# Optimization experiments

Hardware: AMD Instinct MI355X
Metric: run time of the kernel (lower is better)

Reference implementation:

```python
import jax, jax.numpy as jnp
import numpy as np

D = 128
N_A = 50000
N_B = 50000
E = 600000
EPS = 1e-5

def setup_inputs() -> dict:
    key = jax.random.key(0)
    ks = jax.random.split(key, 16)
    s = 1.0 / np.sqrt(D)
    inp = {
        "x_A": jax.random.normal(ks[0], (N_A, D), jnp.float32),
        "x_B": jax.random.normal(ks[1], (N_B, D), jnp.float32),
        "ei_aa": jax.random.randint(ks[2], (2, E), 0, N_A),
        "ei_ba": jnp.stack([jax.random.randint(ks[3], (E,), 0, N_B),
                             jax.random.randint(ks[4], (E,), 0, N_A)]),
        "ei_ab": jnp.stack([jax.random.randint(ks[5], (E,), 0, N_A),
                             jax.random.randint(ks[6], (E,), 0, N_B)]),
        # SAGEConv params per edge type: W_l (neighbor), W_r (root), bias
        "W_l_aa": jax.random.uniform(ks[7], (D, D), jnp.float32, -s, s),
        "W_r_aa": jax.random.uniform(ks[8], (D, D), jnp.float32, -s, s),
        "b_aa": jnp.zeros((D,), jnp.float32),
        "W_l_ba": jax.random.uniform(ks[9], (D, D), jnp.float32, -s, s),
        "W_r_ba": jax.random.uniform(ks[10], (D, D), jnp.float32, -s, s),
        "b_ba": jnp.zeros((D,), jnp.float32),
        "W_l_ab": jax.random.uniform(ks[11], (D, D), jnp.float32, -s, s),
        "W_r_ab": jax.random.uniform(ks[12], (D, D), jnp.float32, -s, s),
        "b_ab": jnp.zeros((D,), jnp.float32),
        "gamma": jnp.ones((D,), jnp.float32),
        "beta": jnp.zeros((D,), jnp.float32),
    }
    return inp

def _sage(x_src, x_dst, ei, W_l, W_r, b, n_dst):
    # mean aggregation of gathered neighbor features (0 for isolated nodes, like PyG)
    msgs = x_src[ei[0]]                                            # [E, D]
    ssum = jax.ops.segment_sum(msgs, ei[1], num_segments=n_dst)    # [n_dst, D]
    cnt = jax.ops.segment_sum(jnp.ones((ei.shape[1], 1), x_src.dtype), ei[1], num_segments=n_dst)
    mean = ssum / jnp.maximum(cnt, 1.0)
    return mean @ W_l.T + x_dst @ W_r.T + b

def _layernorm(x, gamma, beta):
    mu = jnp.mean(x, axis=-1, keepdims=True)
    var = jnp.mean(jnp.square(x - mu), axis=-1, keepdims=True)
    return (x - mu) * jax.lax.rsqrt(var + EPS) * gamma + beta

def reference(x_A, x_B, ei_aa, ei_ba, ei_ab,
              W_l_aa, W_r_aa, b_aa, W_l_ba, W_r_ba, b_ba,
              W_l_ab, W_r_ab, b_ab, gamma, beta):
    # HeteroConv(aggr='sum'): sum conv outputs per destination node type
    out_A = (_sage(x_A, x_A, ei_aa, W_l_aa, W_r_aa, b_aa, N_A)
             + _sage(x_B, x_A, ei_ba, W_l_ba, W_r_ba, b_ba, N_A))
    out_B = _sage(x_A, x_B, ei_ab, W_l_ab, W_r_ab, b_ab, N_B)
    out_A = jax.nn.relu(_layernorm(out_A, gamma, beta))
    out_B = jax.nn.relu(_layernorm(out_B, gamma, beta))
    return out_A, out_B
```

## Files before the change

kernel.cpp:

```cpp
#include <hip/hip_runtime.h>

#define NNODE 50000
#define NEDGE 600000
#define NDST 150000
#define NEALL 1800000
#define NBKT 586
#define EPB 16384
#define P5B 110
#define ECAP 8192

typedef __attribute__((ext_vector_type(8))) __bf16 bf16x8;
typedef __attribute__((ext_vector_type(4))) float f32x4;
typedef __attribute__((ext_vector_type(4))) unsigned int u32x4;

__device__ int dtype_of(const void* gamma) {
    unsigned int g = *(const unsigned int*)gamma;
    if (g == 0x3F803F80u) return 0;
    if (g == 0x3C003C00u) return 1;
    return 2;
}

__device__ float bf2f(unsigned short u) {
    unsigned int x = ((unsigned int)u) << 16;
    float f;
    __builtin_memcpy(&f, &x, 4);
    return f;
}

__device__ float bflo(unsigned int w) {
    unsigned int x = w << 16;
    float f;
    __builtin_memcpy(&f, &x, 4);
    return f;
}
__device__ float bfhi(unsigned int w) {
    unsigned int x = w & 0xFFFF0000u;
    float f;
    __builtin_memcpy(&f, &x, 4);
    return f;
}

__device__ unsigned short f2bf(float f) {
    unsigned int x;
    __builtin_memcpy(&x, &f, 4);
    unsigned int r = (x + 0x7FFFu + ((x >> 16) & 1u)) >> 16;
    return (unsigned short)r;
}

__device__ float ldf(const void* p, int i, int dt) {
    if (dt == 0) return bf2f(((const unsigned short*)p)[i]);
    if (dt == 1) return (float)(((const _Float16*)p)[i]);
    return ((const float*)p)[i];
}

__device__ void stf(void* p, int i, int dt, float v) {
    if (dt == 0) ((unsigned short*)p)[i] = f2bf(v);
    else if (dt == 1) ((_Float16*)p)[i] = (_Float16)v;
    else ((float*)p)[i] = v;
}

__device__ void edge4(const int* ei_aa, const int* ei_ba, const int* ei_ab,
                      int e, int4* d4, int4* s4) {
    const int* dbase;
    const int* sbase;
    int add;
    if (e < NEDGE) { sbase = ei_aa + e; dbase = ei_aa + NEDGE + e; add = 0; }
    else if (e < 2 * NEDGE) {
        int ee = e - NEDGE;
        sbase = ei_ba + ee; dbase = ei_ba + NEDGE + ee; add = 50000;
    } else {
        int ee = e - 2 * NEDGE;
        sbase = ei_ab + ee; dbase = ei_ab + NEDGE + ee; add = 100000;
    }
    int4 d = *(const int4*)dbase;
    d.x += add; d.y += add; d.z += add; d.w += add;
    *d4 = d;
    *s4 = *(const int4*)sbase;
}

__global__ __launch_bounds__(1024) void p5_sort(
    const int* ei_aa, const int* ei_ba, const int* ei_ab,
    unsigned int* blkBuf, int* bbCnt, int* ibOfs) {
    __shared__ int cnt[NBKT];
    __shared__ int ls[1024];
    __shared__ unsigned int buf[EPB];
    int t = threadIdx.x;
    int4 dreg[4], sreg[4];
    bool val[4];
    int e0 = blockIdx.x * EPB + t * 16;
#pragma unroll
    for (int u = 0; u < 4; ++u) {
        int e = e0 + u * 4;
        val[u] = e < NEALL;
        if (val[u]) edge4(ei_aa, ei_ba, ei_ab, e, &dreg[u], &sreg[u]);
    }
    if (t < NBKT) cnt[t] = 0;
    __syncthreads();
#pragma unroll
    for (int u = 0; u < 4; ++u) {
        if (val[u]) {
            atomicAdd(&cnt[dreg[u].x >> 8], 1);
            atomicAdd(&cnt[dreg[u].y >> 8], 1);
            atomicAdd(&cnt[dreg[u].z >> 8], 1);
            atomicAdd(&cnt[dreg[u].w >> 8], 1);
        }
    }
    __syncthreads();
    int v = (t < NBKT) ? cnt[t] : 0;
    ls[t] = v;
    __syncthreads();
    for (int o = 1; o < 1024; o <<= 1) {
        int add = (t >= o) ? ls[t - o] : 0;
        __syncthreads();
        ls[t] += add;
        __syncthreads();
    }
    if (t < NBKT) {
        int excl = ls[t] - v;
        bbCnt[blockIdx.x * NBKT + t] = v;
        ibOfs[blockIdx.x * NBKT + t] = excl;
        cnt[t] = excl;
    }
    __syncthreads();
#pragma unroll
    for (int u = 0; u < 4; ++u) {
        if (val[u]) {
            int dv[4] = {dreg[u].x, dreg[u].y, dreg[u].z, dreg[u].w};
            int sv[4] = {sreg[u].x, sreg[u].y, sreg[u].z, sreg[u].w};
#pragma unroll
            for (int w = 0; w < 4; ++w) {
                int bkt = dv[w] >> 8;
                int r = atomicAdd(&cnt[bkt], 1);
                buf[r] = ((unsigned int)(dv[w] & 255) << 16) | (unsigned int)sv[w];
            }
        }
    }
    __syncthreads();
    unsigned int* dst = blkBuf + blockIdx.x * EPB;
#pragma unroll
    for (int u = 0; u < 4; ++u) {
        int idx = t * 16 + u * 4;
        *(u32x4*)&dst[idx] = *(const u32x4*)&buf[idx];
    }
}

__global__ void p2_colsum(const int* bbCnt, int* colSum) {
    int wave = threadIdx.x >> 6;
    int lane = threadIdx.x & 63;
    int j = blockIdx.x * 4 + wave;
    if (j >= NBKT) return;
    int s = 0;
    if (lane < P5B) s += bbCnt[lane * NBKT + j];
    if (lane + 64 < P5B) s += bbCnt[(lane + 64) * NBKT + j];
    for (int o = 1; o < 64; o <<= 1) s += __shfl_xor(s, o);
    if (lane == 0) colSum[j] = s;
}

__global__ void p3_scan(const int* colSum, int* bucketStart) {
    __shared__ int ls[1024];
    int t = threadIdx.x;
    int v = (t < NBKT) ? colSum[t] : 0;
    ls[t] = v;
    __syncthreads();
    for (int o = 1; o < 1024; o <<= 1) {
        int add = (t >= o) ? ls[t - o] : 0;
        __syncthreads();
        ls[t] += add;
        __syncthreads();
    }
    if (t < NBKT) bucketStart[t] = ls[t] - v;
    if (t == 0) bucketStart[NBKT] = NEALL;
}

__device__ unsigned int rd_entry(const unsigned int* blkBuf, const int* rp,
                                 const int* runSrc, int i) {
    int lo = 0, hi = P5B - 1;
    while (lo < hi) {
        int m = (lo + hi) >> 1;
        if (rp[m] > i) hi = m;
        else lo = m + 1;
    }
    int base = lo ? rp[lo - 1] : 0;
    return blkBuf[runSrc[lo] + (i - base)];
}

__global__ __launch_bounds__(256) void p6_fine(
    const unsigned int* blkBuf, const int* bbCnt, const int* ibOfs,
    const int* bucketStart, int* rowStart, int* edgeSrc) {
    __shared__ int rp[128];
    __shared__ int runSrc[P5B];
    __shared__ unsigned int ebuf[ECAP];
    __shared__ int h[256];
    __shared__ int s[256];
    __shared__ int cur[256];
    int t = threadIdx.x;
    int j = blockIdx.x;
    int lo = bucketStart[j];
    int tot = bucketStart[j + 1] - lo;

    if (t < 128) {
        int c = (t < P5B) ? bbCnt[t * NBKT + j] : 0;
        rp[t] = c;
        if (t < P5B) runSrc[t] = t * EPB + ibOfs[t * NBKT + j];
    }
    __syncthreads();
    for (int o = 1; o < 128; o <<= 1) {
        int add = (t < 128 && t >= o) ? rp[t - o] : 0;
        __syncthreads();
        if (t < 128) rp[t] += add;
        __syncthreads();
    }

    bool staged = tot <= ECAP;
    if (staged) {
        for (int i = t; i < tot; i += 256)
            ebuf[i] = rd_entry(blkBuf, rp, runSrc, i);
    }
    h[t] = 0;
    __syncthreads();
    for (int i = t; i < tot; i += 256) {
        unsigned int w = staged ? ebuf[i] : rd_entry(blkBuf, rp, runSrc, i);
        atomicAdd(&h[w >> 16], 1);
    }
    __syncthreads();
    s[t] = h[t];
    __syncthreads();
    for (int o = 1; o < 256; o <<= 1) {
        int add = (t >= o) ? s[t - o] : 0;
        __syncthreads();
        s[t] += add;
        __syncthreads();
    }
    int excl = s[t] - h[t];
    int dst = j * 256 + t;
    if (dst < NDST) rowStart[dst] = lo + excl;
    if (j == NBKT - 1 && t == 0) rowStart[NDST] = NEALL;
    cur[t] = lo + excl;
    __syncthreads();
    for (int i = t; i < tot; i += 256) {
        unsigned int w = staged ? ebuf[i] : rd_entry(blkBuf, rp, runSrc, i);
        int pos = atomicAdd(&cur[w >> 16], 1);
        edgeSrc[pos] = (int)(w & 0xFFFFu);
    }
}

__global__ __launch_bounds__(256) void gather3_kernel(
    const void* x_A, const void* x_B, const int* rowStart, const int* edgeSrc,
    unsigned short* mean1, unsigned short* mean2, unsigned short* mean3,
    const void* gam) {
    int dt = dtype_of(gam);
    int wave = threadIdx.x >> 6;
    int lane = threadIdx.x & 63;
    int d = blockIdx.x * 4 + wave;
    if (d >= NDST) return;
    const void* x;
    unsigned short* mean;
    int node;
    if (d < 50000) { x = x_A; mean = mean1; node = d; }
    else if (d < 100000) { x = x_B; mean = mean2; node = d - 50000; }
    else { x = x_A; mean = mean3; node = d - 100000; }

    int beg = rowStart[d];
    int end = rowStart[d + 1];

    if (dt == 0) {
        const u32x4* xq = (const u32x4*)x;
        int sub = lane >> 4;
        int col = lane & 15;
        float a[8];
#pragma unroll
        for (int j = 0; j < 8; ++j) a[j] = 0.0f;

        for (int i = beg; i < end; i += 8) {
            int e0 = i + sub;
            int e1 = i + 4 + sub;
            bool p0 = e0 < end;
            bool p1 = e1 < end;
            int s0 = edgeSrc[p0 ? e0 : beg];
            int s1 = edgeSrc[p1 ? e1 : beg];
            u32x4 w0 = xq[s0 * 16 + col];
            u32x4 w1 = xq[s1 * 16 + col];
            if (!p0) w0 = u32x4{0u, 0u, 0u, 0u};
            if (!p1) w1 = u32x4{0u, 0u, 0u, 0u};
            a[0] += bflo(w0.x) + bflo(w1.x);
            a[1] += bfhi(w0.x) + bfhi(w1.x);
            a[2] += bflo(w0.y) + bflo(w1.y);
            a[3] += bfhi(w0.y) + bfhi(w1.y);
            a[4] += bflo(w0.z) + bflo(w1.z);
            a[5] += bfhi(w0.z) + bfhi(w1.z);
            a[6] += bflo(w0.w) + bflo(w1.w);
            a[7] += bfhi(w0.w) + bfhi(w1.w);
        }
#pragma unroll
        for (int j = 0; j < 8; ++j) {
            a[j] += __shfl_xor(a[j], 16);
            a[j] += __shfl_xor(a[j], 32);
        }
        float inv = (end > beg) ? 1.0f / (float)(end - beg) : 0.0f;
        if (lane < 16) {
            u32x4 o;
            o.x = (unsigned int)f2bf(a[0] * inv) | ((unsigned int)f2bf(a[1] * inv) << 16);
            o.y = (unsigned int)f2bf(a[2] * inv) | ((unsigned int)f2bf(a[3] * inv) << 16);
            o.z = (unsigned int)f2bf(a[4] * inv) | ((unsigned int)f2bf(a[5] * inv) << 16);
            o.w = (unsigned int)f2bf(a[6] * inv) | ((unsigned int)f2bf(a[7] * inv) << 16);
            ((u32x4*)mean)[node * 16 + lane] = o;
        }
    } else {
        float a0 = 0.0f, a1 = 0.0f;
        for (int i = beg; i < end; ++i) {
            int src = edgeSrc[i];
            a0 += ldf(x, src * 128 + 2 * lane, dt);
            a1 += ldf(x, src * 128 + 2 * lane + 1, dt);
        }
        float inv = (end > beg) ? 1.0f / (float)(end - beg) : 0.0f;
        unsigned int lo = f2bf(a0 * inv);
        unsigned int hi = f2bf(a1 * inv);
        ((unsigned int*)mean)[node * 64 + lane] = lo | (hi << 16);
    }
}

__global__ void prep_kernel(const void* Wl_aa, const void* Wr_aa, const void* b_aa,
                            const void* Wl_ba, const void* Wr_ba, const void* b_ba,
                            const void* Wl_ab, const void* Wr_ab, const void* b_ab,
                            unsigned short* WA, unsigned short* WB,
                            float* biasA, float* biasB, const void* gam) {
    int dt = dtype_of(gam);
    int idx = blockIdx.x * 256 + threadIdx.x;
    if (idx < 49152) {
        int n = idx / 384;
        int k = idx % 384;
        float v;
        if (k < 128) v = ldf(Wl_aa, n * 128 + k, dt);
        else if (k < 256) v = ldf(Wl_ba, n * 128 + k - 128, dt);
        else v = ldf(Wr_aa, n * 128 + k - 256, dt) + ldf(Wr_ba, n * 128 + k - 256, dt);
        WA[idx] = f2bf(v);
    } else if (idx < 49152 + 32768) {
        int i = idx - 49152;
        int n = i / 256;
        int k = i % 256;
        float v;
        if (k < 128) v = ldf(Wl_ab, n * 128 + k, dt);
        else v = ldf(Wr_ab, n * 128 + k - 128, dt);
        WB[i] = f2bf(v);
    } else if (idx < 49152 + 32768 + 128) {
        int j = idx - (49152 + 32768);
        biasA[j] = ldf(b_aa, j, dt) + ldf(b_ba, j, dt);
    } else if (idx < 49152 + 32768 + 256) {
        int j = idx - (49152 + 32768 + 128);
        biasB[j] = ldf(b_ab, j, dt);
    }
}

__device__ bf16x8 pack8(const float* f) {
    unsigned short u[8];
    for (int j = 0; j < 8; ++j) u[j] = f2bf(f[j]);
    bf16x8 r;
    __builtin_memcpy(&r, u, 16);
    return r;
}

template <int KTOT>
__device__ bf16x8 loadA(const unsigned short* mean1, const unsigned short* mean2,
                        const void* x, int r, int k, int dt) {
    if (k < 128) {
        return *(const bf16x8*)(mean1 + r * 128 + k);
    }
    if (KTOT == 384 && k < 256) {
        return *(const bf16x8*)(mean2 + r * 128 + (k - 128));
    }
    int kx = k - (KTOT - 128);
    if (dt == 0) {
        return *(const bf16x8*)((const unsigned short*)x + r * 128 + kx);
    }
    float f[8];
    for (int j = 0; j < 8; ++j) f[j] = ldf(x, r * 128 + kx + j, dt);
    return pack8(f);
}

template <int KTOT>
__device__ void gemm_body(int bx, const unsigned short* mean1,
                          const unsigned short* mean2, const void* x,
                          const unsigned short* Wu, const float* bias,
                          const void* gam, const void* bet, void* out,
                          int rowOff, int dt) {
    int lane = threadIdx.x & 63;
    int wave = threadIdx.x >> 6;
    int q16 = lane >> 4;
    int l16 = lane & 15;
    int mBase = (bx * 4 + wave) * 32;

    int r0 = mBase + l16;
    int r1 = mBase + 16 + l16;
    if (r0 > NNODE - 1) r0 = NNODE - 1;
    if (r1 > NNODE - 1) r1 = NNODE - 1;

    f32x4 acc[2][8];
    for (int rt = 0; rt < 2; ++rt)
        for (int tt = 0; tt < 8; ++tt) acc[rt][tt] = f32x4{0.f, 0.f, 0.f, 0.f};

    const int NCH = KTOT / 32;
    for (int ck = 0; ck < NCH; ++ck) {
        int k = ck * 32 + q16 * 8;
        bf16x8 a0 = loadA<KTOT>(mean1, mean2, x, r0, k, dt);
        bf16x8 a1 = loadA<KTOT>(mean1, mean2, x, r1, k, dt);
#pragma unroll
        for (int tt = 0; tt < 8; ++tt) {
            int n = tt * 16 + l16;
            bf16x8 b = *(const bf16x8*)(Wu + n * KTOT + k);
            acc[0][tt] = __builtin_amdgcn_mfma_f32_16x16x32_bf16(a0, b, acc[0][tt], 0, 0, 0);
            acc[1][tt] = __builtin_amdgcn_mfma_f32_16x16x32_bf16(a1, b, acc[1][tt], 0, 0, 0);
        }
    }

    float g[8], be[8], bs[8];
    for (int tt = 0; tt < 8; ++tt) {
        int j = tt * 16 + l16;
        g[tt] = ldf(gam, j, dt);
        be[tt] = ldf(bet, j, dt);
        bs[tt] = bias[j];
    }

    for (int rt = 0; rt < 2; ++rt) {
        for (int q = 0; q < 4; ++q) {
            int row = mBase + rt * 16 + q16 * 4 + q;
            float v[8];
            float s = 0.f, ss = 0.f;
            for (int tt = 0; tt < 8; ++tt) {
                v[tt] = acc[rt][tt][q] + bs[tt];
                s += v[tt];
                ss += v[tt] * v[tt];
            }
            for (int off = 1; off <= 8; off <<= 1) {
                s += __shfl_xor(s, off);
                ss += __shfl_xor(ss, off);
            }
            float m = s * (1.0f / 128.0f);
            float var = ss * (1.0f / 128.0f) - m * m;
            float rstd = rsqrtf(var + 1e-5f);
            if (row < NNODE) {
                for (int tt = 0; tt < 8; ++tt) {
                    float o = (v[tt] - m) * rstd * g[tt] + be[tt];
                    if (o < 0.0f) o = 0.0f;
                    stf(out, (rowOff + row) * 128 + tt * 16 + l16, dt, o);
                }
            }
        }
    }
}

__global__ __launch_bounds__(256) void gemm_ln_all(
    const unsigned short* mean1, const unsigned short* mean2,
    const unsigned short* mean3, const void* x_A, const void* x_B,
    const unsigned short* WA, const unsigned short* WB,
    const float* bA, const float* bB,
    const void* gam, const void* bet, void* out) {
    int dt = dtype_of(gam);
    if (blockIdx.x < 391)
        gemm_body<384>(blockIdx.x, mean1, mean2, x_A, WA, bA, gam, bet, out, 0, dt);
    else
        gemm_body<256>(blockIdx.x - 391, mean3, nullptr, x_B, WB, bB, gam, bet, out,
                       NNODE, dt);
}

extern "C" void kernel_launch(void* const* d_in, const int* in_sizes, int n_in,
                              void* d_out, int out_size, void* d_ws, size_t ws_size,
                              hipStream_t stream) {
    const void* x_A = d_in[0];
    const void* x_B = d_in[1];
    const int* ei_aa = (const int*)d_in[2];
    const int* ei_ba = (const int*)d_in[3];
    const int* ei_ab = (const int*)d_in[4];
    const void* W_l_aa = d_in[5];
    const void* W_r_aa = d_in[6];
    const void* b_aa = d_in[7];
    const void* W_l_ba = d_in[8];
    const void* W_r_ba = d_in[9];
    const void* b_ba = d_in[10];
    const void* W_l_ab = d_in[11];
    const void* W_r_ab = d_in[12];
    const void* b_ab = d_in[13];
    const void* gam = d_in[14];
    const void* bet = d_in[15];

    unsigned short* mean1 = (unsigned short*)d_ws;
    unsigned short* mean2 = mean1 + 6400000;
    unsigned short* mean3 = mean2 + 6400000;
    unsigned short* WA = mean3 + 6400000;
    unsigned short* WB = WA + 49152;
    float* bA = (float*)(WB + 32768);
    float* bB = bA + 128;
    int* bbCnt = (int*)(bB + 128);
    int* ibOfs = bbCnt + P5B * NBKT;
    int* colSum = ibOfs + P5B * NBKT;
    int* bucketStart = colSum + NBKT;
    int* rowStart = bucketStart + NBKT + 1;
    int* edgeSrc = rowStart + NDST + 1;
    unsigned int* blkBuf = (unsigned int*)mean1;

    prep_kernel<<<322, 256, 0, stream>>>(W_l_aa, W_r_aa, b_aa, W_l_ba, W_r_ba, b_ba,
                                         W_l_ab, W_r_ab, b_ab, WA, WB, bA, bB, gam);

    p5_sort<<<P5B, 1024, 0, stream>>>(ei_aa, ei_ba, ei_ab, blkBuf, bbCnt, ibOfs);
    p2_colsum<<<147, 256, 0, stream>>>(bbCnt, colSum);
    p3_scan<<<1, 1024, 0, stream>>>(colSum, bucketStart);
    p6_fine<<<NBKT, 256, 0, stream>>>(blkBuf, bbCnt, ibOfs, bucketStart,
                                      rowStart, edgeSrc);

    gather3_kernel<<<37500, 256, 0, stream>>>(x_A, x_B, rowStart, edgeSrc,
                                              mean1, mean2, mean3, gam);

    gemm_ln_all<<<782, 256, 0, stream>>>(mean1, mean2, mean3, x_A, x_B,
                                         WA, WB, bA, bB, gam, bet, d_out);
}
```

Measured before the change: 461.1 us.

## Fuse neighbor-mean gather into GEMM+LayerNorm via LDS, merge colsum into scan

```diff
diff --git a/kernel.cpp b/kernel.cpp
--- a/kernel.cpp
+++ b/kernel.cpp
@@ -8,6 +8,8 @@
 #define EPB 16384
 #define P5B 110
 #define ECAP 8192
+#define NPB 128
+#define FBN 391
 
 typedef __attribute__((ext_vector_type(8))) __bf16 bf16x8;
 typedef __attribute__((ext_vector_type(4))) float f32x4;
@@ -144,22 +146,13 @@
     }
 }
 
-__global__ void p2_colsum(const int* bbCnt, int* colSum) {
-    int wave = threadIdx.x >> 6;
-    int lane = threadIdx.x & 63;
-    int j = blockIdx.x * 4 + wave;
-    if (j >= NBKT) return;
-    int s = 0;
-    if (lane < P5B) s += bbCnt[lane * NBKT + j];
-    if (lane + 64 < P5B) s += bbCnt[(lane + 64) * NBKT + j];
-    for (int o = 1; o < 64; o <<= 1) s += __shfl_xor(s, o);
-    if (lane == 0) colSum[j] = s;
-}
-
-__global__ void p3_scan(const int* colSum, int* bucketStart) {
+__global__ void p23_scan(const int* bbCnt, int* bucketStart) {
     __shared__ int ls[1024];
     int t = threadIdx.x;
-    int v = (t < NBKT) ? colSum[t] : 0;
+    int v = 0;
+    if (t < NBKT) {
+        for (int b = 0; b < P5B; ++b) v += bbCnt[b * NBKT + t];
+    }
     ls[t] = v;
     __syncthreads();
     for (int o = 1; o < 1024; o <<= 1) {
@@ -241,81 +234,6 @@
         unsigned int w = staged ? ebuf[i] : rd_entry(blkBuf, rp, runSrc, i);
         int pos = atomicAdd(&cur[w >> 16], 1);
         edgeSrc[pos] = (int)(w & 0xFFFFu);
-    }
-}
-
-__global__ __launch_bounds__(256) void gather3_kernel(
-    const void* x_A, const void* x_B, const int* rowStart, const int* edgeSrc,
-    unsigned short* mean1, unsigned short* mean2, unsigned short* mean3,
-    const void* gam) {
-    int dt = dtype_of(gam);
-    int wave = threadIdx.x >> 6;
-    int lane = threadIdx.x & 63;
-    int d = blockIdx.x * 4 + wave;
-    if (d >= NDST) return;
-    const void* x;
-    unsigned short* mean;
-    int node;
-    if (d < 50000) { x = x_A; mean = mean1; node = d; }
-    else if (d < 100000) { x = x_B; mean = mean2; node = d - 50000; }
-    else { x = x_A; mean = mean3; node = d - 100000; }
-
-    int beg = rowStart[d];
-    int end = rowStart[d + 1];
-
-    if (dt == 0) {
-        const u32x4* xq = (const u32x4*)x;
-        int sub = lane >> 4;
-        int col = lane & 15;
-        float a[8];
-#pragma unroll
-        for (int j = 0; j < 8; ++j) a[j] = 0.0f;
-
-        for (int i = beg; i < end; i += 8) {
-            int e0 = i + sub;
-            int e1 = i + 4 + sub;
-            bool p0 = e0 < end;
-            bool p1 = e1 < end;
-            int s0 = edgeSrc[p0 ? e0 : beg];
-            int s1 = edgeSrc[p1 ? e1 : beg];
-            u32x4 w0 = xq[s0 * 16 + col];
-            u32x4 w1 = xq[s1 * 16 + col];
-            if (!p0) w0 = u32x4{0u, 0u, 0u, 0u};
-            if (!p1) w1 = u32x4{0u, 0u, 0u, 0u};
-            a[0] += bflo(w0.x) + bflo(w1.x);
-            a[1] += bfhi(w0.x) + bfhi(w1.x);
-            a[2] += bflo(w0.y) + bflo(w1.y);
-            a[3] += bfhi(w0.y) + bfhi(w1.y);
-            a[4] += bflo(w0.z) + bflo(w1.z);
-            a[5] += bfhi(w0.z) + bfhi(w1.z);
-            a[6] += bflo(w0.w) + bflo(w1.w);
-            a[7] += bfhi(w0.w) + bfhi(w1.w);
-        }
-#pragma unroll
-        for (int j = 0; j < 8; ++j) {
-            a[j] += __shfl_xor(a[j], 16);
-            a[j] += __shfl_xor(a[j], 32);
-        }
-        float inv = (end > beg) ? 1.0f / (float)(end - beg) : 0.0f;
-        if (lane < 16) {
-            u32x4 o;
-            o.x = (unsigned int)f2bf(a[0] * inv) | ((unsigned int)f2bf(a[1] * inv) << 16);
-            o.y = (unsigned int)f2bf(a[2] * inv) | ((unsigned int)f2bf(a[3] * inv) << 16);
-            o.z = (unsigned int)f2bf(a[4] * inv) | ((unsigned int)f2bf(a[5] * inv) << 16);
-            o.w = (unsigned int)f2bf(a[6] * inv) | ((unsigned int)f2bf(a[7] * inv) << 16);
-            ((u32x4*)mean)[node * 16 + lane] = o;
-        }
-    } else {
-        float a0 = 0.0f, a1 = 0.0f;
-        for (int i = beg; i < end; ++i) {
-            int src = edgeSrc[i];
-            a0 += ldf(x, src * 128 + 2 * lane, dt);
-            a1 += ldf(x, src * 128 + 2 * lane + 1, dt);
-        }
-        float inv = (end > beg) ? 1.0f / (float)(end - beg) : 0.0f;
-        unsigned int lo = f2bf(a0 * inv);
-        unsigned int hi = f2bf(a1 * inv);
-        ((unsigned int*)mean)[node * 64 + lane] = lo | (hi << 16);
     }
 }
 
@@ -360,59 +278,51 @@
 }
 
 template <int KTOT>
-__device__ bf16x8 loadA(const unsigned short* mean1, const unsigned short* mean2,
-                        const void* x, int r, int k, int dt) {
-    if (k < 128) {
-        return *(const bf16x8*)(mean1 + r * 128 + k);
-    }
-    if (KTOT == 384 && k < 256) {
-        return *(const bf16x8*)(mean2 + r * 128 + (k - 128));
-    }
-    int kx = k - (KTOT - 128);
-    if (dt == 0) {
-        return *(const bf16x8*)((const unsigned short*)x + r * 128 + kx);
-    }
-    float f[8];
-    for (int j = 0; j < 8; ++j) f[j] = ldf(x, r * 128 + kx + j, dt);
-    return pack8(f);
-}
-
-template <int KTOT>
-__device__ void gemm_body(int bx, const unsigned short* mean1,
-                          const unsigned short* mean2, const void* x,
-                          const unsigned short* Wu, const float* bias,
-                          const void* gam, const void* bet, void* out,
-                          int rowOff, int dt) {
+__device__ void fused_gemm(const unsigned short* meanLds, const void* x,
+                           const unsigned short* Wu, const float* bias,
+                           const void* gam, const void* bet, void* out,
+                           int n0, int rowOff, int dt) {
+    const int KMEAN = KTOT - 128;
     int lane = threadIdx.x & 63;
     int wave = threadIdx.x >> 6;
     int q16 = lane >> 4;
     int l16 = lane & 15;
-    int mBase = (bx * 4 + wave) * 32;
-
-    int r0 = mBase + l16;
-    int r1 = mBase + 16 + l16;
-    if (r0 > NNODE - 1) r0 = NNODE - 1;
-    if (r1 > NNODE - 1) r1 = NNODE - 1;
-
-    f32x4 acc[2][8];
-    for (int rt = 0; rt < 2; ++rt)
-        for (int tt = 0; tt < 8; ++tt) acc[rt][tt] = f32x4{0.f, 0.f, 0.f, 0.f};
+    int rL = wave * 16 + l16;
+    int xrow = n0 + rL;
+    if (xrow > NNODE - 1) xrow = NNODE - 1;
+
+    f32x4 acc[8];
+#pragma unroll
+    for (int tt = 0; tt < 8; ++tt) acc[tt] = f32x4{0.f, 0.f, 0.f, 0.f};
 
     const int NCH = KTOT / 32;
+#pragma unroll
     for (int ck = 0; ck < NCH; ++ck) {
         int k = ck * 32 + q16 * 8;
-        bf16x8 a0 = loadA<KTOT>(mean1, mean2, x, r0, k, dt);
-        bf16x8 a1 = loadA<KTOT>(mean1, mean2, x, r1, k, dt);
+        bf16x8 a0;
+        if (k < KMEAN) {
+            int bo = (rL * 512 + k * 2) ^ ((rL & 7) << 4);
+            a0 = *(const bf16x8*)((const char*)meanLds + bo);
+        } else {
+            int kx = k - KMEAN;
+            if (dt == 0) {
+                a0 = *(const bf16x8*)((const unsigned short*)x + xrow * 128 + kx);
+            } else {
+                float f[8];
+                for (int j = 0; j < 8; ++j) f[j] = ldf(x, xrow * 128 + kx + j, dt);
+                a0 = pack8(f);
+            }
+        }
 #pragma unroll
         for (int tt = 0; tt < 8; ++tt) {
             int n = tt * 16 + l16;
             bf16x8 b = *(const bf16x8*)(Wu + n * KTOT + k);
-            acc[0][tt] = __builtin_amdgcn_mfma_f32_16x16x32_bf16(a0, b, acc[0][tt], 0, 0, 0);
-            acc[1][tt] = __builtin_amdgcn_mfma_f32_16x16x32_bf16(a1, b, acc[1][tt], 0, 0, 0);
+            acc[tt] = __builtin_amdgcn_mfma_f32_16x16x32_bf16(a0, b, acc[tt], 0, 0, 0);
         }
     }
 
     float g[8], be[8], bs[8];
+#pragma unroll
     for (int tt = 0; tt < 8; ++tt) {
         int j = tt * 16 + l16;
         g[tt] = ldf(gam, j, dt);
@@ -420,46 +330,129 @@
         bs[tt] = bias[j];
     }
 
-    for (int rt = 0; rt < 2; ++rt) {
-        for (int q = 0; q < 4; ++q) {
-            int row = mBase + rt * 16 + q16 * 4 + q;
-            float v[8];
-            float s = 0.f, ss = 0.f;
+    for (int q = 0; q < 4; ++q) {
+        int rowL = wave * 16 + q16 * 4 + q;
+        float v[8];
+        float s = 0.f, ss = 0.f;
+#pragma unroll
+        for (int tt = 0; tt < 8; ++tt) {
+            v[tt] = acc[tt][q] + bs[tt];
+            s += v[tt];
+            ss += v[tt] * v[tt];
+        }
+        for (int off = 1; off <= 8; off <<= 1) {
+            s += __shfl_xor(s, off);
+            ss += __shfl_xor(ss, off);
+        }
+        float m = s * (1.0f / 128.0f);
+        float var = ss * (1.0f / 128.0f) - m * m;
+        float rstd = rsqrtf(var + 1e-5f);
+        int grow = n0 + rowL;
+        if (grow < NNODE) {
+#pragma unroll
             for (int tt = 0; tt < 8; ++tt) {
-                v[tt] = acc[rt][tt][q] + bs[tt];
-                s += v[tt];
-                ss += v[tt] * v[tt];
+                float o = (v[tt] - m) * rstd * g[tt] + be[tt];
+                if (o < 0.0f) o = 0.0f;
+                stf(out, (rowOff + grow) * 128 + tt * 16 + l16, dt, o);
             }
-            for (int off = 1; off <= 8; off <<= 1) {
-                s += __shfl_xor(s, off);
-                ss += __shfl_xor(ss, off);
-            }
-            float m = s * (1.0f / 128.0f);
-            float var = ss * (1.0f / 128.0f) - m * m;
-            float rstd = rsqrtf(var + 1e-5f);
-            if (row < NNODE) {
-                for (int tt = 0; tt < 8; ++tt) {
-                    float o = (v[tt] - m) * rstd * g[tt] + be[tt];
-                    if (o < 0.0f) o = 0.0f;
-                    stf(out, (rowOff + row) * 128 + tt * 16 + l16, dt, o);
-                }
-            }
-        }
-    }
-}
-
-__global__ __launch_bounds__(256) void gemm_ln_all(
-    const unsigned short* mean1, const unsigned short* mean2,
-    const unsigned short* mean3, const void* x_A, const void* x_B,
+        }
+    }
+}
+
+__global__ __launch_bounds__(512, 4) void fused_gg(
+    const void* x_A, const void* x_B, const int* rowStart, const int* edgeSrc,
     const unsigned short* WA, const unsigned short* WB,
     const float* bA, const float* bB,
     const void* gam, const void* bet, void* out) {
+    __shared__ unsigned short meanLds[NPB * 256];
     int dt = dtype_of(gam);
-    if (blockIdx.x < 391)
-        gemm_body<384>(blockIdx.x, mean1, mean2, x_A, WA, bA, gam, bet, out, 0, dt);
+    bool typeB = blockIdx.x >= FBN;
+    int bx = typeB ? blockIdx.x - FBN : blockIdx.x;
+    int n0 = bx * NPB;
+    int wave = threadIdx.x >> 6;
+    int lane = threadIdx.x & 63;
+    int sub = lane >> 4;
+    int col = lane & 15;
+
+    int nlists = typeB ? NPB : 2 * NPB;
+    for (int L = wave; L < nlists; L += 8) {
+        int node, part, dstIdx, row;
+        const void* x;
+        if (!typeB) {
+            node = n0 + (L >> 1);
+            part = L & 1;
+            dstIdx = part ? 50000 + node : node;
+            x = part ? x_B : x_A;
+            row = L >> 1;
+        } else {
+            node = n0 + L;
+            part = 0;
+            dstIdx = 100000 + node;
+            x = x_A;
+            row = L;
+        }
+
+        float a[8];
+#pragma unroll
+        for (int j = 0; j < 8; ++j) a[j] = 0.0f;
+        int deg = 0;
+        if (node < NNODE) {
+            int beg = rowStart[dstIdx];
+            int end = rowStart[dstIdx + 1];
+            deg = end - beg;
+            if (dt == 0) {
+                const u32x4* xq = (const u32x4*)x;
+                for (int i = beg; i < end; i += 8) {
+                    int e0 = i + sub;
+                    int e1 = i + 4 + sub;
+                    bool p0 = e0 < end;
+                    bool p1 = e1 < end;
+                    int s0 = edgeSrc[p0 ? e0 : beg];
+                    int s1 = edgeSrc[p1 ? e1 : beg];
+                    u32x4 w0 = xq[s0 * 16 + col];
+                    u32x4 w1 = xq[s1 * 16 + col];
+                    if (!p0) w0 = u32x4{0u, 0u, 0u, 0u};
+                    if (!p1) w1 = u32x4{0u, 0u, 0u, 0u};
+                    a[0] += bflo(w0.x) + bflo(w1.x);
+                    a[1] += bfhi(w0.x) + bfhi(w1.x);
+                    a[2] += bflo(w0.y) + bflo(w1.y);
+                    a[3] += bfhi(w0.y) + bfhi(w1.y);
+                    a[4] += bflo(w0.z) + bflo(w1.z);
+                    a[5] += bfhi(w0.z) + bfhi(w1.z);
+                    a[6] += bflo(w0.w) + bflo(w1.w);
+                    a[7] += bfhi(w0.w) + bfhi(w1.w);
+                }
+            } else {
+                for (int i = beg + sub; i < end; i += 4) {
+                    int src = edgeSrc[i];
+#pragma unroll
+                    for (int j = 0; j < 8; ++j)
+                        a[j] += ldf(x, src * 128 + col * 8 + j, dt);
+                }
+            }
+        }
+#pragma unroll
+        for (int j = 0; j < 8; ++j) {
+            a[j] += __shfl_xor(a[j], 16);
+            a[j] += __shfl_xor(a[j], 32);
+        }
+        float inv = (deg > 0) ? 1.0f / (float)deg : 0.0f;
+        if (lane < 16) {
+            u32x4 o;
+            o.x = (unsigned int)f2bf(a[0] * inv) | ((unsigned int)f2bf(a[1] * inv) << 16);
+            o.y = (unsigned int)f2bf(a[2] * inv) | ((unsigned int)f2bf(a[3] * inv) << 16);
+            o.z = (unsigned int)f2bf(a[4] * inv) | ((unsigned int)f2bf(a[5] * inv) << 16);
+            o.w = (unsigned int)f2bf(a[6] * inv) | ((unsigned int)f2bf(a[7] * inv) << 16);
+            int byteOff = (row * 512 + part * 256 + col * 16) ^ ((row & 7) << 4);
+            *(u32x4*)((char*)meanLds + byteOff) = o;
+        }
+    }
+    __syncthreads();
+
+    if (!typeB)
+        fused_gemm<384>(meanLds, x_A, WA, bA, gam, bet, out, n0, 0, dt);
     else
-        gemm_body<256>(blockIdx.x - 391, mean3, nullptr, x_B, WB, bB, gam, bet, out,
-                       NNODE, dt);
+        fused_gemm<256>(meanLds, x_B, WB, bB, gam, bet, out, n0, NNODE, dt);
 }
 
 extern "C" void kernel_launch(void* const* d_in, const int* in_sizes, int n_in,
@@ -482,33 +475,25 @@
     const void* gam = d_in[14];
     const void* bet = d_in[15];
 
-    unsigned short* mean1 = (unsigned short*)d_ws;
-    unsigned short* mean2 = mean1 + 6400000;
-    unsigned short* mean3 = mean2 + 6400000;
-    unsigned short* WA = mean3 + 6400000;
+    int* bbCnt = (int*)d_ws;
+    int* ibOfs = bbCnt + P5B * NBKT;
+    int* bucketStart = ibOfs + P5B * NBKT;
+    int* rowStart = bucketStart + NBKT + 1;
+    int* edgeSrc = rowStart + NDST + 1;
+    unsigned int* blkBuf = (unsigned int*)(edgeSrc + NEALL);
+    unsigned short* WA = (unsigned short*)(blkBuf + P5B * EPB);
     unsigned short* WB = WA + 49152;
     float* bA = (float*)(WB + 32768);
     float* bB = bA + 128;
-    int* bbCnt = (int*)(bB + 128);
-    int* ibOfs = bbCnt + P5B * NBKT;
-    int* colSum = ibOfs + P5B * NBKT;
-    int* bucketStart = colSum + NBKT;
-    int* rowStart = bucketStart + NBKT + 1;
-    int* edgeSrc = rowStart + NDST + 1;
-    unsigned int* blkBuf = (unsigned int*)mean1;
 
     prep_kernel<<<322, 256, 0, stream>>>(W_l_aa, W_r_aa, b_aa, W_l_ba, W_r_ba, b_ba,
                                          W_l_ab, W_r_ab, b_ab, WA, WB, bA, bB, gam);
 
     p5_sort<<<P5B, 1024, 0, stream>>>(ei_aa, ei_ba, ei_ab, blkBuf, bbCnt, ibOfs);
-    p2_colsum<<<147, 256, 0, stream>>>(bbCnt, colSum);
-    p3_scan<<<1, 1024, 0, stream>>>(colSum, bucketStart);
+    p23_scan<<<1, 1024, 0, stream>>>(bbCnt, bucketStart);
     p6_fine<<<NBKT, 256, 0, stream>>>(blkBuf, bbCnt, ibOfs, bucketStart,
                                       rowStart, edgeSrc);
 
-    gather3_kernel<<<37500, 256, 0, stream>>>(x_A, x_B, rowStart, edgeSrc,
-                                              mean1, mean2, mean3, gam);
-
-    gemm_ln_all<<<782, 256, 0, stream>>>(mean1, mean2, mean3, x_A, x_B,
-                                         WA, WB, bA, bB, gam, bet, d_out);
-}
+    fused_gg<<<2 * FBN, 512, 0, stream>>>(x_A, x_B, rowStart, edgeSrc,
+                                          WA, WB, bA, bB, gam, bet, d_out);
+}
```

Result: slower. 782.4 us (+69.7%).

## Fuse fine sort with neighbor gather and fold weight prep into coarse sort

Applied to the files above, without the earlier changes.

```diff
diff --git a/kernel.cpp b/kernel.cpp
--- a/kernel.cpp
+++ b/kernel.cpp
@@ -4,10 +4,12 @@
 #define NEDGE 600000
 #define NDST 150000
 #define NEALL 1800000
-#define NBKT 586
-#define EPB 16384
-#define P5B 110
-#define ECAP 8192
+#define BSZ 147
+#define NBKT 1021
+#define EPB 8192
+#define P5B 220
+#define PREPB 81
+#define ECAP 3072
 
 typedef __attribute__((ext_vector_type(8))) __bf16 bf16x8;
 typedef __attribute__((ext_vector_type(4))) float f32x4;
@@ -78,254 +80,11 @@
     *s4 = *(const int4*)sbase;
 }
 
-__global__ __launch_bounds__(1024) void p5_sort(
-    const int* ei_aa, const int* ei_ba, const int* ei_ab,
-    unsigned int* blkBuf, int* bbCnt, int* ibOfs) {
-    __shared__ int cnt[NBKT];
-    __shared__ int ls[1024];
-    __shared__ unsigned int buf[EPB];
-    int t = threadIdx.x;
-    int4 dreg[4], sreg[4];
-    bool val[4];
-    int e0 = blockIdx.x * EPB + t * 16;
-#pragma unroll
-    for (int u = 0; u < 4; ++u) {
-        int e = e0 + u * 4;
-        val[u] = e < NEALL;
-        if (val[u]) edge4(ei_aa, ei_ba, ei_ab, e, &dreg[u], &sreg[u]);
-    }
-    if (t < NBKT) cnt[t] = 0;
-    __syncthreads();
-#pragma unroll
-    for (int u = 0; u < 4; ++u) {
-        if (val[u]) {
-            atomicAdd(&cnt[dreg[u].x >> 8], 1);
-            atomicAdd(&cnt[dreg[u].y >> 8], 1);
-            atomicAdd(&cnt[dreg[u].z >> 8], 1);
-            atomicAdd(&cnt[dreg[u].w >> 8], 1);
-        }
-    }
-    __syncthreads();
-    int v = (t < NBKT) ? cnt[t] : 0;
-    ls[t] = v;
-    __syncthreads();
-    for (int o = 1; o < 1024; o <<= 1) {
-        int add = (t >= o) ? ls[t - o] : 0;
-        __syncthreads();
-        ls[t] += add;
-        __syncthreads();
-    }
-    if (t < NBKT) {
-        int excl = ls[t] - v;
-        bbCnt[blockIdx.x * NBKT + t] = v;
-        ibOfs[blockIdx.x * NBKT + t] = excl;
-        cnt[t] = excl;
-    }
-    __syncthreads();
-#pragma unroll
-    for (int u = 0; u < 4; ++u) {
-        if (val[u]) {
-            int dv[4] = {dreg[u].x, dreg[u].y, dreg[u].z, dreg[u].w};
-            int sv[4] = {sreg[u].x, sreg[u].y, sreg[u].z, sreg[u].w};
-#pragma unroll
-            for (int w = 0; w < 4; ++w) {
-                int bkt = dv[w] >> 8;
-                int r = atomicAdd(&cnt[bkt], 1);
-                buf[r] = ((unsigned int)(dv[w] & 255) << 16) | (unsigned int)sv[w];
-            }
-        }
-    }
-    __syncthreads();
-    unsigned int* dst = blkBuf + blockIdx.x * EPB;
-#pragma unroll
-    for (int u = 0; u < 4; ++u) {
-        int idx = t * 16 + u * 4;
-        *(u32x4*)&dst[idx] = *(const u32x4*)&buf[idx];
-    }
-}
-
-__global__ void p2_colsum(const int* bbCnt, int* colSum) {
-    int wave = threadIdx.x >> 6;
-    int lane = threadIdx.x & 63;
-    int j = blockIdx.x * 4 + wave;
-    if (j >= NBKT) return;
-    int s = 0;
-    if (lane < P5B) s += bbCnt[lane * NBKT + j];
-    if (lane + 64 < P5B) s += bbCnt[(lane + 64) * NBKT + j];
-    for (int o = 1; o < 64; o <<= 1) s += __shfl_xor(s, o);
-    if (lane == 0) colSum[j] = s;
-}
-
-__global__ void p3_scan(const int* colSum, int* bucketStart) {
-    __shared__ int ls[1024];
-    int t = threadIdx.x;
-    int v = (t < NBKT) ? colSum[t] : 0;
-    ls[t] = v;
-    __syncthreads();
-    for (int o = 1; o < 1024; o <<= 1) {
-        int add = (t >= o) ? ls[t - o] : 0;
-        __syncthreads();
-        ls[t] += add;
-        __syncthreads();
-    }
-    if (t < NBKT) bucketStart[t] = ls[t] - v;
-    if (t == 0) bucketStart[NBKT] = NEALL;
-}
-
-__device__ unsigned int rd_entry(const unsigned int* blkBuf, const int* rp,
-                                 const int* runSrc, int i) {
-    int lo = 0, hi = P5B - 1;
-    while (lo < hi) {
-        int m = (lo + hi) >> 1;
-        if (rp[m] > i) hi = m;
-        else lo = m + 1;
-    }
-    int base = lo ? rp[lo - 1] : 0;
-    return blkBuf[runSrc[lo] + (i - base)];
-}
-
-__global__ __launch_bounds__(256) void p6_fine(
-    const unsigned int* blkBuf, const int* bbCnt, const int* ibOfs,
-    const int* bucketStart, int* rowStart, int* edgeSrc) {
-    __shared__ int rp[128];
-    __shared__ int runSrc[P5B];
-    __shared__ unsigned int ebuf[ECAP];
-    __shared__ int h[256];
-    __shared__ int s[256];
-    __shared__ int cur[256];
-    int t = threadIdx.x;
-    int j = blockIdx.x;
-    int lo = bucketStart[j];
-    int tot = bucketStart[j + 1] - lo;
-
-    if (t < 128) {
-        int c = (t < P5B) ? bbCnt[t * NBKT + j] : 0;
-        rp[t] = c;
-        if (t < P5B) runSrc[t] = t * EPB + ibOfs[t * NBKT + j];
-    }
-    __syncthreads();
-    for (int o = 1; o < 128; o <<= 1) {
-        int add = (t < 128 && t >= o) ? rp[t - o] : 0;
-        __syncthreads();
-        if (t < 128) rp[t] += add;
-        __syncthreads();
-    }
-
-    bool staged = tot <= ECAP;
-    if (staged) {
-        for (int i = t; i < tot; i += 256)
-            ebuf[i] = rd_entry(blkBuf, rp, runSrc, i);
-    }
-    h[t] = 0;
-    __syncthreads();
-    for (int i = t; i < tot; i += 256) {
-        unsigned int w = staged ? ebuf[i] : rd_entry(blkBuf, rp, runSrc, i);
-        atomicAdd(&h[w >> 16], 1);
-    }
-    __syncthreads();
-    s[t] = h[t];
-    __syncthreads();
-    for (int o = 1; o < 256; o <<= 1) {
-        int add = (t >= o) ? s[t - o] : 0;
-        __syncthreads();
-        s[t] += add;
-        __syncthreads();
-    }
-    int excl = s[t] - h[t];
-    int dst = j * 256 + t;
-    if (dst < NDST) rowStart[dst] = lo + excl;
-    if (j == NBKT - 1 && t == 0) rowStart[NDST] = NEALL;
-    cur[t] = lo + excl;
-    __syncthreads();
-    for (int i = t; i < tot; i += 256) {
-        unsigned int w = staged ? ebuf[i] : rd_entry(blkBuf, rp, runSrc, i);
-        int pos = atomicAdd(&cur[w >> 16], 1);
-        edgeSrc[pos] = (int)(w & 0xFFFFu);
-    }
-}
-
-__global__ __launch_bounds__(256) void gather3_kernel(
-    const void* x_A, const void* x_B, const int* rowStart, const int* edgeSrc,
-    unsigned short* mean1, unsigned short* mean2, unsigned short* mean3,
-    const void* gam) {
-    int dt = dtype_of(gam);
-    int wave = threadIdx.x >> 6;
-    int lane = threadIdx.x & 63;
-    int d = blockIdx.x * 4 + wave;
-    if (d >= NDST) return;
-    const void* x;
-    unsigned short* mean;
-    int node;
-    if (d < 50000) { x = x_A; mean = mean1; node = d; }
-    else if (d < 100000) { x = x_B; mean = mean2; node = d - 50000; }
-    else { x = x_A; mean = mean3; node = d - 100000; }
-
-    int beg = rowStart[d];
-    int end = rowStart[d + 1];
-
-    if (dt == 0) {
-        const u32x4* xq = (const u32x4*)x;
-        int sub = lane >> 4;
-        int col = lane & 15;
-        float a[8];
-#pragma unroll
-        for (int j = 0; j < 8; ++j) a[j] = 0.0f;
-
-        for (int i = beg; i < end; i += 8) {
-            int e0 = i + sub;
-            int e1 = i + 4 + sub;
-            bool p0 = e0 < end;
-            bool p1 = e1 < end;
-            int s0 = edgeSrc[p0 ? e0 : beg];
-            int s1 = edgeSrc[p1 ? e1 : beg];
-            u32x4 w0 = xq[s0 * 16 + col];
-            u32x4 w1 = xq[s1 * 16 + col];
-            if (!p0) w0 = u32x4{0u, 0u, 0u, 0u};
-            if (!p1) w1 = u32x4{0u, 0u, 0u, 0u};
-            a[0] += bflo(w0.x) + bflo(w1.x);
-            a[1] += bfhi(w0.x) + bfhi(w1.x);
-            a[2] += bflo(w0.y) + bflo(w1.y);
-            a[3] += bfhi(w0.y) + bfhi(w1.y);
-            a[4] += bflo(w0.z) + bflo(w1.z);
-            a[5] += bfhi(w0.z) + bfhi(w1.z);
-            a[6] += bflo(w0.w) + bflo(w1.w);
-            a[7] += bfhi(w0.w) + bfhi(w1.w);
-        }
-#pragma unroll
-        for (int j = 0; j < 8; ++j) {
-            a[j] += __shfl_xor(a[j], 16);
-            a[j] += __shfl_xor(a[j], 32);
-        }
-        float inv = (end > beg) ? 1.0f / (float)(end - beg) : 0.0f;
-        if (lane < 16) {
-            u32x4 o;
-            o.x = (unsigned int)f2bf(a[0] * inv) | ((unsigned int)f2bf(a[1] * inv) << 16);
-            o.y = (unsigned int)f2bf(a[2] * inv) | ((unsigned int)f2bf(a[3] * inv) << 16);
-            o.z = (unsigned int)f2bf(a[4] * inv) | ((unsigned int)f2bf(a[5] * inv) << 16);
-            o.w = (unsigned int)f2bf(a[6] * inv) | ((unsigned int)f2bf(a[7] * inv) << 16);
-            ((u32x4*)mean)[node * 16 + lane] = o;
-        }
-    } else {
-        float a0 = 0.0f, a1 = 0.0f;
-        for (int i = beg; i < end; ++i) {
-            int src = edgeSrc[i];
-            a0 += ldf(x, src * 128 + 2 * lane, dt);
-            a1 += ldf(x, src * 128 + 2 * lane + 1, dt);
-        }
-        float inv = (end > beg) ? 1.0f / (float)(end - beg) : 0.0f;
-        unsigned int lo = f2bf(a0 * inv);
-        unsigned int hi = f2bf(a1 * inv);
-        ((unsigned int*)mean)[node * 64 + lane] = lo | (hi << 16);
-    }
-}
-
-__global__ void prep_kernel(const void* Wl_aa, const void* Wr_aa, const void* b_aa,
-                            const void* Wl_ba, const void* Wr_ba, const void* b_ba,
-                            const void* Wl_ab, const void* Wr_ab, const void* b_ab,
-                            unsigned short* WA, unsigned short* WB,
-                            float* biasA, float* biasB, const void* gam) {
-    int dt = dtype_of(gam);
-    int idx = blockIdx.x * 256 + threadIdx.x;
+__device__ void prep_body(int idx, const void* Wl_aa, const void* Wr_aa,
+                          const void* b_aa, const void* Wl_ba, const void* Wr_ba,
+                          const void* b_ba, const void* Wl_ab, const void* Wr_ab,
+                          const void* b_ab, unsigned short* WA, unsigned short* WB,
+                          float* biasA, float* biasB, int dt) {
     if (idx < 49152) {
         int n = idx / 384;
         int k = idx % 384;
@@ -351,6 +110,264 @@
     }
 }
 
+__global__ __launch_bounds__(1024) void p5_sort(
+    const int* ei_aa, const int* ei_ba, const int* ei_ab,
+    unsigned int* blkBuf, int* bbCnt, int* ibOfs,
+    const void* Wl_aa, const void* Wr_aa, const void* b_aa,
+    const void* Wl_ba, const void* Wr_ba, const void* b_ba,
+    const void* Wl_ab, const void* Wr_ab, const void* b_ab,
+    unsigned short* WA, unsigned short* WB,
+    float* biasA, float* biasB, const void* gam) {
+    int t = threadIdx.x;
+    if (blockIdx.x >= P5B) {
+        int dt = dtype_of(gam);
+        int idx = (blockIdx.x - P5B) * 1024 + t;
+        prep_body(idx, Wl_aa, Wr_aa, b_aa, Wl_ba, Wr_ba, b_ba,
+                  Wl_ab, Wr_ab, b_ab, WA, WB, biasA, biasB, dt);
+        return;
+    }
+    __shared__ int cnt[NBKT];
+    __shared__ int ls[1024];
+    __shared__ unsigned int buf[EPB];
+    int4 dreg[2], sreg[2];
+    bool val[2];
+    int e0 = blockIdx.x * EPB + t * 8;
+#pragma unroll
+    for (int u = 0; u < 2; ++u) {
+        int e = e0 + u * 4;
+        val[u] = e < NEALL;
+        if (val[u]) edge4(ei_aa, ei_ba, ei_ab, e, &dreg[u], &sreg[u]);
+    }
+    if (t < NBKT) cnt[t] = 0;
+    __syncthreads();
+#pragma unroll
+    for (int u = 0; u < 2; ++u) {
+        if (val[u]) {
+            atomicAdd(&cnt[dreg[u].x / BSZ], 1);
+            atomicAdd(&cnt[dreg[u].y / BSZ], 1);
+            atomicAdd(&cnt[dreg[u].z / BSZ], 1);
+            atomicAdd(&cnt[dreg[u].w / BSZ], 1);
+        }
+    }
+    __syncthreads();
+    int v = (t < NBKT) ? cnt[t] : 0;
+    ls[t] = v;
+    __syncthreads();
+    for (int o = 1; o < 1024; o <<= 1) {
+        int add = (t >= o) ? ls[t - o] : 0;
+        __syncthreads();
+        ls[t] += add;
+        __syncthreads();
+    }
+    if (t < NBKT) {
+        int excl = ls[t] - v;
+        bbCnt[blockIdx.x * NBKT + t] = v;
+        ibOfs[blockIdx.x * NBKT + t] = excl;
+        cnt[t] = excl;
+    }
+    __syncthreads();
+#pragma unroll
+    for (int u = 0; u < 2; ++u) {
+        if (val[u]) {
+            int dv[4] = {dreg[u].x, dreg[u].y, dreg[u].z, dreg[u].w};
+            int sv[4] = {sreg[u].x, sreg[u].y, sreg[u].z, sreg[u].w};
+#pragma unroll
+            for (int w = 0; w < 4; ++w) {
+                int bkt = dv[w] / BSZ;
+                int dl = dv[w] - bkt * BSZ;
+                int r = atomicAdd(&cnt[bkt], 1);
+                buf[r] = ((unsigned int)dl << 16) | (unsigned int)sv[w];
+            }
+        }
+    }
+    __syncthreads();
+    unsigned int* dst = blkBuf + blockIdx.x * EPB;
+#pragma unroll
+    for (int u = 0; u < 2; ++u) {
+        int idx = t * 8 + u * 4;
+        *(u32x4*)&dst[idx] = *(const u32x4*)&buf[idx];
+    }
+}
+
+__global__ __launch_bounds__(512, 8) void p6g_kernel(
+    const unsigned int* blkBuf, const int* bbCnt, const int* ibOfs,
+    const void* x_A, const void* x_B,
+    unsigned short* mean1, unsigned short* mean2, unsigned short* mean3,
+    const void* gam) {
+    __shared__ int rp[256];
+    __shared__ int runSrc[P5B];
+    __shared__ unsigned int ebuf[ECAP];
+    __shared__ unsigned short ebuf2[ECAP];
+    __shared__ int rowLds[BSZ + 1];
+    __shared__ int h[BSZ];
+    __shared__ int cur[BSZ];
+    __shared__ int sc[256];
+    int t = threadIdx.x;
+    int j = blockIdx.x;
+    int dt = dtype_of(gam);
+    int wave = t >> 6;
+    int lane = t & 63;
+
+    if (t < 256) {
+        int c = (t < P5B) ? bbCnt[t * NBKT + j] : 0;
+        rp[t] = c;
+        if (t < P5B) runSrc[t] = t * EPB + ibOfs[t * NBKT + j];
+    }
+    __syncthreads();
+    for (int o = 1; o < 256; o <<= 1) {
+        int add = (t < 256 && t >= o) ? rp[t - o] : 0;
+        __syncthreads();
+        if (t < 256) rp[t] += add;
+        __syncthreads();
+    }
+    int tot = rp[P5B - 1];
+    bool staged = tot <= ECAP;
+
+    if (staged) {
+        for (int r = wave; r < P5B; r += 8) {
+            int base = r ? rp[r - 1] : 0;
+            int n = rp[r] - base;
+            int gs = runSrc[r];
+            for (int k = lane; k < n; k += 64)
+                ebuf[base + k] = blkBuf[gs + k];
+        }
+    }
+    if (t < BSZ) h[t] = 0;
+    __syncthreads();
+    if (staged) {
+        for (int i = t; i < tot; i += 512)
+            atomicAdd(&h[(int)(ebuf[i] >> 16)], 1);
+    } else {
+        for (int r = wave; r < P5B; r += 8) {
+            int base = r ? rp[r - 1] : 0;
+            int n = rp[r] - base;
+            int gs = runSrc[r];
+            for (int k = lane; k < n; k += 64)
+                atomicAdd(&h[(int)(blkBuf[gs + k] >> 16)], 1);
+        }
+    }
+    __syncthreads();
+    if (t < 256) sc[t] = (t < BSZ) ? h[t] : 0;
+    __syncthreads();
+    for (int o = 1; o < 256; o <<= 1) {
+        int add = (t < 256 && t >= o) ? sc[t - o] : 0;
+        __syncthreads();
+        if (t < 256) sc[t] += add;
+        __syncthreads();
+    }
+    if (t < BSZ) {
+        int excl = sc[t] - h[t];
+        rowLds[t] = excl;
+        cur[t] = excl;
+    }
+    if (t == 0) rowLds[BSZ] = tot;
+    __syncthreads();
+    if (staged) {
+        for (int i = t; i < tot; i += 512) {
+            unsigned int w = ebuf[i];
+            int pos = atomicAdd(&cur[(int)(w >> 16)], 1);
+            ebuf2[pos] = (unsigned short)(w & 0xFFFFu);
+        }
+    }
+    __syncthreads();
+
+    int sub = lane >> 4;
+    int col = lane & 15;
+    for (int dl = wave; dl < BSZ; dl += 8) {
+        int d = j * BSZ + dl;
+        if (d >= NDST) break;
+        const void* x;
+        unsigned short* mean;
+        int node;
+        if (d < 50000) { x = x_A; mean = mean1; node = d; }
+        else if (d < 100000) { x = x_B; mean = mean2; node = d - 50000; }
+        else { x = x_A; mean = mean3; node = d - 100000; }
+
+        if (!staged) {
+            float b0 = 0.f, b1 = 0.f;
+            int deg = 0;
+            for (int r = 0; r < P5B; ++r) {
+                int base = r ? rp[r - 1] : 0;
+                int n = rp[r] - base;
+                int gs = runSrc[r];
+                for (int k = 0; k < n; ++k) {
+                    unsigned int w = blkBuf[gs + k];
+                    if ((int)(w >> 16) == dl) {
+                        int src = (int)(w & 0xFFFFu);
+                        if (dt == 0) {
+                            unsigned int vv = ((const unsigned int*)x)[src * 64 + lane];
+                            b0 += bflo(vv);
+                            b1 += bfhi(vv);
+                        } else {
+                            b0 += ldf(x, src * 128 + 2 * lane, dt);
+                            b1 += ldf(x, src * 128 + 2 * lane + 1, dt);
+                        }
+                        ++deg;
+                    }
+                }
+            }
+            float inv = deg ? 1.0f / (float)deg : 0.0f;
+            ((unsigned int*)mean)[node * 64 + lane] =
+                (unsigned int)f2bf(b0 * inv) | ((unsigned int)f2bf(b1 * inv) << 16);
+            continue;
+        }
+
+        int beg = rowLds[dl];
+        int end = rowLds[dl + 1];
+
+        if (dt == 0) {
+            const u32x4* xq = (const u32x4*)x;
+            float a[8];
+#pragma unroll
+            for (int q = 0; q < 8; ++q) a[q] = 0.0f;
+            for (int i = beg; i < end; i += 8) {
+                int e0 = i + sub;
+                int e1 = i + 4 + sub;
+                bool p0 = e0 < end;
+                bool p1 = e1 < end;
+                int s0 = ebuf2[p0 ? e0 : beg];
+                int s1 = ebuf2[p1 ? e1 : beg];
+                u32x4 w0 = xq[s0 * 16 + col];
+                u32x4 w1 = xq[s1 * 16 + col];
+                if (!p0) w0 = u32x4{0u, 0u, 0u, 0u};
+                if (!p1) w1 = u32x4{0u, 0u, 0u, 0u};
+                a[0] += bflo(w0.x) + bflo(w1.x);
+                a[1] += bfhi(w0.x) + bfhi(w1.x);
+                a[2] += bflo(w0.y) + bflo(w1.y);
+                a[3] += bfhi(w0.y) + bfhi(w1.y);
+                a[4] += bflo(w0.z) + bflo(w1.z);
+                a[5] += bfhi(w0.z) + bfhi(w1.z);
+                a[6] += bflo(w0.w) + bflo(w1.w);
+                a[7] += bfhi(w0.w) + bfhi(w1.w);
+            }
+#pragma unroll
+            for (int q = 0; q < 8; ++q) {
+                a[q] += __shfl_xor(a[q], 16);
+                a[q] += __shfl_xor(a[q], 32);
+            }
+            float inv = (end > beg) ? 1.0f / (float)(end - beg) : 0.0f;
+            if (lane < 16) {
+                u32x4 o;
+                o.x = (unsigned int)f2bf(a[0] * inv) | ((unsigned int)f2bf(a[1] * inv) << 16);
+                o.y = (unsigned int)f2bf(a[2] * inv) | ((unsigned int)f2bf(a[3] * inv) << 16);
+                o.z = (unsigned int)f2bf(a[4] * inv) | ((unsigned int)f2bf(a[5] * inv) << 16);
+                o.w = (unsigned int)f2bf(a[6] * inv) | ((unsigned int)f2bf(a[7] * inv) << 16);
+                ((u32x4*)mean)[node * 16 + lane] = o;
+            }
+        } else {
+            float b0 = 0.f, b1 = 0.f;
+            for (int i = beg; i < end; ++i) {
+                int src = ebuf2[i];
+                b0 += ldf(x, src * 128 + 2 * lane, dt);
+                b1 += ldf(x, src * 128 + 2 * lane + 1, dt);
+            }
+            float inv = (end > beg) ? 1.0f / (float)(end - beg) : 0.0f;
+            ((unsigned int*)mean)[node * 64 + lane] =
+                (unsigned int)f2bf(b0 * inv) | ((unsigned int)f2bf(b1 * inv) << 16);
+        }
+    }
+}
+
 __device__ bf16x8 pack8(const float* f) {
     unsigned short u[8];
     for (int j = 0; j < 8; ++j) u[j] = f2bf(f[j]);
@@ -482,32 +499,24 @@
     const void* gam = d_in[14];
     const void* bet = d_in[15];
 
-    unsigned short* mean1 = (unsigned short*)d_ws;
+    int* bbCnt = (int*)d_ws;
+    int* ibOfs = bbCnt + P5B * NBKT;
+    unsigned int* blkBuf = (unsigned int*)(ibOfs + P5B * NBKT);
+    unsigned short* mean1 = (unsigned short*)(blkBuf + P5B * EPB);
     unsigned short* mean2 = mean1 + 6400000;
     unsigned short* mean3 = mean2 + 6400000;
     unsigned short* WA = mean3 + 6400000;
     unsigned short* WB = WA + 49152;
     float* bA = (float*)(WB + 32768);
     float* bB = bA + 128;
-    int* bbCnt = (int*)(bB + 128);
-    int* ibOfs = bbCnt + P5B * NBKT;
-    int* colSum = ibOfs + P5B * NBKT;
-    int* bucketStart = colSum + NBKT;
-    int* rowStart = bucketStart + NBKT + 1;
-    int* edgeSrc = rowStart + NDST + 1;
-    unsigned int* blkBuf = (unsigned int*)mean1;
-
-    prep_kernel<<<322, 256, 0, stream>>>(W_l_aa, W_r_aa, b_aa, W_l_ba, W_r_ba, b_ba,
-                                         W_l_ab, W_r_ab, b_ab, WA, WB, bA, bB, gam);
-
-    p5_sort<<<P5B, 1024, 0, stream>>>(ei_aa, ei_ba, ei_ab, blkBuf, bbCnt, ibOfs);
-    p2_colsum<<<147, 256, 0, stream>>>(bbCnt, colSum);
-    p3_scan<<<1, 1024, 0, stream>>>(colSum, bucketStart);
-    p6_fine<<<NBKT, 256, 0, stream>>>(blkBuf, bbCnt, ibOfs, bucketStart,
-                                      rowStart, edgeSrc);
-
-    gather3_kernel<<<37500, 256, 0, stream>>>(x_A, x_B, rowStart, edgeSrc,
-                                              mean1, mean2, mean3, gam);
+
+    p5_sort<<<P5B + PREPB, 1024, 0, stream>>>(
+        ei_aa, ei_ba, ei_ab, blkBuf, bbCnt, ibOfs,
+        W_l_aa, W_r_aa, b_aa, W_l_ba, W_r_ba, b_ba,
+        W_l_ab, W_r_ab, b_ab, WA, WB, bA, bB, gam);
+
+    p6g_kernel<<<NBKT, 512, 0, stream>>>(blkBuf, bbCnt, ibOfs, x_A, x_B,
+                                         mean1, mean2, mean3, gam);
 
     gemm_ln_all<<<782, 256, 0, stream>>>(mean1, mean2, mean3, x_A, x_B,
                                          WA, WB, bA, bB, gam, bet, d_out);
```

Measured after the change: 369.6 us. 19.8% less time.
